# Performance work log

Measured on AMD Instinct MI355X. Metric: run time of the kernel, lower is better.

The kernel has to match this reference:

```python
import jax, jax.numpy as jnp
import numpy as np

N = 100000      # nodes
E = 3200000     # directed edges
G = 1024        # graphs in batch


def setup_inputs() -> dict:
    key = jax.random.key(0)
    ks = jax.random.split(key, 12)
    x = jax.random.normal(ks[0], (N, 4), dtype=jnp.float32)
    edge_index = jax.random.randint(ks[1], (2, E), 0, N, dtype=jnp.int64)
    batch = jnp.sort(jax.random.randint(ks[2], (N,), 0, G, dtype=jnp.int64))
    s = 0.1
    return {
        'x': x, 'edge_index': edge_index, 'batch': batch,
        'W_emb': jax.random.normal(ks[3], (4, 1), jnp.float32) * s,
        'b_emb': jax.random.normal(ks[4], (4,), jnp.float32) * s,
        'W1': jax.random.normal(ks[5], (16, 7), jnp.float32) * s,
        'b1': jax.random.normal(ks[6], (16,), jnp.float32) * s,
        'W2': jax.random.normal(ks[7], (8, 16), jnp.float32) * s,
        'b2': jax.random.normal(ks[8], (8,), jnp.float32) * s,
        'W3': jax.random.normal(ks[9], (1, 8), jnp.float32) * s,
        'b3': jax.random.normal(ks[10], (1,), jnp.float32) * s,
    }


def _gcn_norm(edge_index, n):
    # add self-loops (PyG GCNConv default)
    loops = jnp.arange(n, dtype=edge_index.dtype)
    row = jnp.concatenate([edge_index[0], loops])  # source
    col = jnp.concatenate([edge_index[1], loops])  # target
    deg = jax.ops.segment_sum(jnp.ones_like(col, dtype=jnp.float32), col, num_segments=n)
    dinv = jnp.where(deg > 0, deg ** -0.5, 0.0)
    norm = dinv[row] * dinv[col]
    return row, col, norm


def _gcn_conv(h, W, b, row, col, norm, n):
    h = h @ W.T                                   # [n, out]
    msg = h[row] * norm[:, None]                  # gather + scale
    out = jax.ops.segment_sum(msg, col, num_segments=n)
    return out + b


def reference(x, edge_index, batch, W_emb, b_emb, W1, b1, W2, b2, W3, b3):
    row, col, norm = _gcn_norm(edge_index, N)
    atoms_vector = x[:, :1]
    atoms_xyz = x[:, 1:]
    one_hot_emb = atoms_vector @ W_emb.T + b_emb          # [N, 4]
    h = jnp.concatenate([one_hot_emb, atoms_xyz], axis=1) # [N, 7]
    h = jnp.tanh(_gcn_conv(h, W1, b1, row, col, norm, N)) # [N, 16]
    # dropout is identity in eval mode
    h = jnp.tanh(_gcn_conv(h, W2, b2, row, col, norm, N)) # [N, 8]
    # scatter-mean readout over graphs
    sums = jax.ops.segment_sum(h, batch, num_segments=G)
    cnts = jax.ops.segment_sum(jnp.ones((h.shape[0],), h.dtype), batch, num_segments=G)
    pooled = sums / jnp.maximum(cnts, 1.0)[:, None]       # [G, 8]
    return pooled @ W3.T + b3                             # [G, 1]
```

## Files before the change

kernel.cpp:

```cpp
#include <hip/hip_runtime.h>
#include <hip/hip_fp16.h>


constexpr int BLK  = 256;
constexpr int NPB  = 256;
constexpr int NBMX = 512;
constexpr int CAPB = 9216;
constexpr int PBLK = 512;
constexpr int CAPS = 6144;
constexpr int EPT  = 12;
constexpr int SBLK = 512;
constexpr int NIT4 = 5;
constexpr float S8 = 64.0f;

__global__ void k_place(const int4* __restrict__ row4, const int4* __restrict__ col4,
                        int* __restrict__ bucketCnt, unsigned int* __restrict__ data,
                        int E, int NB) {
    __shared__ unsigned int stage[CAPS];
    __shared__ int pos[NBMX], sstart[NBMX], lbase[NBMX];
    __shared__ int wsum[8];
    int t = threadIdx.x;
    int lane = t & 63, w = t >> 6;
    int begin = blockIdx.x * CAPS;
    int end = min(E, begin + CAPS);
    int csize = end - begin;
    int q0 = begin >> 2, q1 = end >> 2;
    if (t < NBMX) pos[t] = 0;
    __syncthreads();
    unsigned int ent[EPT];
    int meta[EPT];
#pragma unroll
    for (int it = 0; it < EPT / 4; it++) {
        int i = q0 + t + it * PBLK;
        bool ok = i < q1;
        int4 c = ok ? col4[i] : make_int4(0, 0, 0, 0);
        int4 r = ok ? row4[i] : make_int4(0, 0, 0, 0);
#pragma unroll
        for (int k = 0; k < 4; k++) {
            int cc = ((const int*)&c)[k];
            int rr = ((const int*)&r)[k];
            int b = cc >> 8;
            int o = ok ? atomicAdd(&pos[b], 1) : 0;
            ent[it * 4 + k] = ((unsigned int)(cc & 255) << 17) | (unsigned int)rr;
            meta[it * 4 + k] = ok ? ((b << 13) | o) : -1;
        }
    }
    __syncthreads();
    int v = pos[t];
    int sc = v;
#pragma unroll
    for (int off = 1; off < 64; off <<= 1) {
        int o = __shfl_up(sc, off, 64);
        if (lane >= off) sc += o;
    }
    if (lane == 63) wsum[w] = sc;
    __syncthreads();
    int pre = 0;
#pragma unroll
    for (int i = 0; i < 8; i++) if (i < w) pre += wsum[i];
    int excl = sc + pre - v;
    sstart[t] = excl;
    lbase[t] = v ? atomicAdd(&bucketCnt[t], v) : 0;
    __syncthreads();
#pragma unroll
    for (int k = 0; k < EPT; k++) {
        int m = meta[k];
        if (m >= 0) stage[sstart[m >> 13] + (m & 0x1FFF)] = ent[k];
    }
    __syncthreads();
    for (int k = t; k < csize; k += PBLK) {
        int lo = 0, hi = NB - 1;
        while (lo < hi) { int m = (lo + hi + 1) >> 1; if (sstart[m] <= k) lo = m; else hi = m - 1; }
        data[(unsigned int)lo * CAPB + (unsigned int)(lbase[lo] + (k - sstart[lo]))] = stage[k];
    }
}

__global__ void k_sort_node1(unsigned int* __restrict__ data,
                             const int* __restrict__ bucketCnt,
                             const float4* __restrict__ x,
                             const float* __restrict__ Wemb, const float* __restrict__ bemb,
                             const float* __restrict__ W1,
                             int* __restrict__ rs, int* __restrict__ re,
                             float* __restrict__ dinv, uint4* __restrict__ u1q, int n) {
    __shared__ int pos[NPB], startl[NPB];
    __shared__ int wsum[4];
    int b = blockIdx.x;
    int t = threadIdx.x;
    int base = b * CAPB;
    int cnt = min(bucketCnt[b], CAPB);
    if (t < NPB) pos[t] = 0;
    __syncthreads();
    const uint4* data4 = (const uint4*)(data + base);
    unsigned int ent[NIT4 * 4];
    int off[NIT4 * 4];
#pragma unroll
    for (int it = 0; it < NIT4; it++) {
        int i4 = t + it * SBLK;
        int i = i4 * 4;
        uint4 p4 = (i < cnt) ? data4[i4] : make_uint4(0, 0, 0, 0);
#pragma unroll
        for (int k = 0; k < 4; k++) {
            int idx = it * 4 + k;
            if (i + k < cnt) {
                unsigned int p = ((const unsigned int*)&p4)[k];
                int dloc = (int)(p >> 17);
                int o = atomicAdd(&pos[dloc], 1);
                ent[idx] = p & 0x1FFFF;
                off[idx] = (dloc << 14) | o;
            } else off[idx] = -1;
        }
    }
    __syncthreads();
    int node = b * NPB + t;
    float d = 0.0f;
    if (t < NPB) {
        int lane = t & 63, w = t >> 6;
        int v = pos[t];
        int sc = v;
#pragma unroll
        for (int o = 1; o < 64; o <<= 1) {
            int s = __shfl_up(sc, o, 64);
            if (lane >= o) sc += s;
        }
        if (lane == 63) wsum[w] = sc;
        __syncthreads();
        int pre = 0;
#pragma unroll
        for (int i = 0; i < 4; i++) if (i < w) pre += wsum[i];
        int excl = sc + pre - v;
        startl[t] = excl;
        if (node < n) {
            rs[node] = base + excl;
            re[node] = base + excl + v;
            d = rsqrtf((float)v + 1.0f);
            dinv[node] = d;
        }
    } else {
        __syncthreads();
    }
    __syncthreads();
#pragma unroll
    for (int it = 0; it < NIT4 * 4; it++) {
        int m = off[it];
        if (m >= 0) data[base + startl[m >> 14] + (m & 0x3FFF)] = ent[it];
    }
    if (t < NPB && node < n) {
        float4 xi = x[node];
        float h0[7];
#pragma unroll
        for (int j = 0; j < 4; j++) h0[j] = xi.x * Wemb[j] + bemb[j];
        h0[4] = xi.y; h0[5] = xi.z; h0[6] = xi.w;
        float s[16];
#pragma unroll
        for (int f = 0; f < 16; f++) {
            float tt = 0.0f;
#pragma unroll
            for (int j = 0; j < 7; j++) tt += h0[j] * W1[f * 7 + j];
            s[f] = tt * d * S8;
        }
        unsigned int w0, w1, w2, w3;
        w0 = __builtin_amdgcn_cvt_pk_fp8_f32(s[0],  s[1],  0,  false);
        w0 = __builtin_amdgcn_cvt_pk_fp8_f32(s[2],  s[3],  w0, true);
        w1 = __builtin_amdgcn_cvt_pk_fp8_f32(s[4],  s[5],  0,  false);
        w1 = __builtin_amdgcn_cvt_pk_fp8_f32(s[6],  s[7],  w1, true);
        w2 = __builtin_amdgcn_cvt_pk_fp8_f32(s[8],  s[9],  0,  false);
        w2 = __builtin_amdgcn_cvt_pk_fp8_f32(s[10], s[11], w2, true);
        w3 = __builtin_amdgcn_cvt_pk_fp8_f32(s[12], s[13], 0,  false);
        w3 = __builtin_amdgcn_cvt_pk_fp8_f32(s[14], s[15], w3, true);
        u1q[node] = make_uint4(w0, w1, w2, w3);
    }
}

typedef float vfloat2 __attribute__((vector_size(8)));

__device__ __forceinline__ void dec16_add(uint4 q, float* acc) {
#pragma unroll
    for (int w = 0; w < 4; w++) {
        unsigned int u = ((const unsigned int*)&q)[w];
        vfloat2 lo = __builtin_amdgcn_cvt_pk_f32_fp8(u, false);
        vfloat2 hi = __builtin_amdgcn_cvt_pk_f32_fp8(u, true);
        acc[4 * w + 0] += lo[0]; acc[4 * w + 1] += lo[1];
        acc[4 * w + 2] += hi[0]; acc[4 * w + 3] += hi[1];
    }
}

__global__ void k_agg1(const unsigned int* __restrict__ sorted,
                       const int* __restrict__ rs, const int* __restrict__ re,
                       const uint4* __restrict__ u1q, const float* __restrict__ dinv,
                       const float* __restrict__ b1, const float* __restrict__ W2,
                       uint4* __restrict__ u2q, int n) {
    int node = blockIdx.x * BLK + threadIdx.x;
    if (node >= n) return;
    int s = rs[node], e = re[node];
    float acc[16];
#pragma unroll
    for (int k = 0; k < 16; k++) acc[k] = 0.0f;
    int i = s;
    for (; i + 4 <= e; i += 4) {
        uint4 q0 = u1q[sorted[i]];
        uint4 q1 = u1q[sorted[i + 1]];
        uint4 q2 = u1q[sorted[i + 2]];
        uint4 q3 = u1q[sorted[i + 3]];
        dec16_add(q0, acc);
        dec16_add(q1, acc);
        dec16_add(q2, acc);
        dec16_add(q3, acc);
    }
    for (; i < e; i++) {
        uint4 q = u1q[sorted[i]];
        dec16_add(q, acc);
    }
    uint4 qs = u1q[node];
    dec16_add(qs, acc);
    float d = dinv[node];
    float dS = d * (1.0f / S8);
    float h1[16];
#pragma unroll
    for (int k = 0; k < 16; k++) h1[k] = tanhf(dS * acc[k] + b1[k]);
    float r[8];
#pragma unroll
    for (int g = 0; g < 8; g++) {
        float tt = 0.0f;
#pragma unroll
        for (int k = 0; k < 16; k++) tt += h1[k] * W2[g * 16 + k];
        r[g] = tt * d;
    }
    union { __half2 h2[4]; uint4 u4; } pk;
#pragma unroll
    for (int q = 0; q < 4; q++) pk.h2[q] = __floats2half2_rn(r[2 * q], r[2 * q + 1]);
    u2q[node] = pk.u4;
}

__global__ void k_agg2_pool(const unsigned int* __restrict__ sorted,
                            const int* __restrict__ rs, const int* __restrict__ re,
                            const uint4* __restrict__ u2q, const float* __restrict__ dinv,
                            const float* __restrict__ b2, const int* __restrict__ batch,
                            float* __restrict__ pooled, float* __restrict__ cnt, int n) {
    int node = blockIdx.x * BLK + threadIdx.x;
    int lane = threadIdx.x & 63;
    bool valid = node < n;
    float h[8];
#pragma unroll
    for (int k = 0; k < 8; k++) h[k] = 0.0f;
    int g = -1;
    if (valid) {
        int s = rs[node], e = re[node];
        float acc[8];
#pragma unroll
        for (int k = 0; k < 8; k++) acc[k] = 0.0f;
        int i = s;
        for (; i + 2 <= e; i += 2) {
            uint4 q0 = u2q[sorted[i]];
            uint4 q1 = u2q[sorted[i + 1]];
            const __half2* p0 = (const __half2*)&q0;
            const __half2* p1 = (const __half2*)&q1;
#pragma unroll
            for (int k = 0; k < 4; k++) {
                float2 a0 = __half22float2(p0[k]);
                float2 a1 = __half22float2(p1[k]);
                acc[2*k]   += a0.x + a1.x;
                acc[2*k+1] += a0.y + a1.y;
            }
        }
        if (i < e) {
            uint4 q = u2q[sorted[i]];
            const __half2* p = (const __half2*)&q;
#pragma unroll
            for (int k = 0; k < 4; k++) {
                float2 a = __half22float2(p[k]);
                acc[2*k]   += a.x;
                acc[2*k+1] += a.y;
            }
        }
        uint4 qs = u2q[node];
        const __half2* ps = (const __half2*)&qs;
        float d = dinv[node];
#pragma unroll
        for (int k = 0; k < 4; k++) {
            float2 a = __half22float2(ps[k]);
            h[2*k]   = tanhf(d * (acc[2*k]   + a.x) + b2[2*k]);
            h[2*k+1] = tanhf(d * (acc[2*k+1] + a.y) + b2[2*k+1]);
        }
        g = batch[node];
    }
    float c = valid ? 1.0f : 0.0f;
#pragma unroll
    for (int off = 1; off < 64; off <<= 1) {
        int gn = __shfl_down(g, off, 64);
        float cn = __shfl_down(c, off, 64);
        float hn[8];
#pragma unroll
        for (int k = 0; k < 8; k++) hn[k] = __shfl_down(h[k], off, 64);
        bool take = (lane + off < 64) && (gn == g);
        if (take) {
            c += cn;
#pragma unroll
            for (int k = 0; k < 8; k++) h[k] += hn[k];
        }
    }
    int gprev = __shfl_up(g, 1, 64);
    bool head = valid && (lane == 0 || gprev != g);
    if (head) {
#pragma unroll
        for (int k = 0; k < 8; k++) atomicAdd(&pooled[g * 8 + k], h[k]);
        atomicAdd(&cnt[g], c);
    }
}

__global__ void k_out(const float* __restrict__ pooled, const float* __restrict__ cnt,
                      const float* __restrict__ W3, const float* __restrict__ b3,
                      float* __restrict__ out, int G) {
    int g = blockIdx.x * BLK + threadIdx.x;
    if (g >= G) return;
    float c = fmaxf(cnt[g], 1.0f);
    float t = 0.0f;
#pragma unroll
    for (int k = 0; k < 8; k++) t += pooled[g * 8 + k] * W3[k];
    out[g] = t / c + b3[0];
}

extern "C" void kernel_launch(void* const* d_in, const int* in_sizes, int n_in,
                              void* d_out, int out_size, void* d_ws, size_t ws_size,
                              hipStream_t stream) {
    const float* x    = (const float*)d_in[0];
    const int*   ei   = (const int*)d_in[1];
    const int*   batch= (const int*)d_in[2];
    const float* Wemb = (const float*)d_in[3];
    const float* bemb = (const float*)d_in[4];
    const float* W1   = (const float*)d_in[5];
    const float* b1   = (const float*)d_in[6];
    const float* W2   = (const float*)d_in[7];
    const float* b2   = (const float*)d_in[8];
    const float* W3   = (const float*)d_in[9];
    const float* b3   = (const float*)d_in[10];
    float* out = (float*)d_out;

    const int n = in_sizes[2];
    const int E = in_sizes[1] / 2;
    const int G = out_size;
    const int* row = ei;
    const int* col = ei + E;
    const int NB = (n + NPB - 1) / NPB;

    float* ws    = (float*)d_ws;
    float* dinv  = ws;
    uint4* u1q   = (uint4*)(ws + n);
    __half* u2h  = (__half*)(ws + 9 * n);
    int* rs      = (int*)(ws + 13 * n);
    int* re      = rs + n;
    int* bucketCnt = re + n;
    float* pooled  = (float*)(bucketCnt + NBMX);
    float* cnt     = pooled + 8 * G;
    unsigned int* data = (unsigned int*)(cnt + G);

    int gridP = (E + CAPS - 1) / CAPS;

    hipMemsetAsync(bucketCnt, 0, (NBMX + 8 * G + G) * sizeof(int), stream);
    k_place<<<gridP, PBLK, 0, stream>>>((const int4*)row, (const int4*)col,
                                        bucketCnt, data, E, NB);
    k_sort_node1<<<NB, SBLK, 0, stream>>>(data, bucketCnt, (const float4*)x,
                                          Wemb, bemb, W1, rs, re, dinv, u1q, n);
    k_agg1<<<(n + BLK - 1) / BLK, BLK, 0, stream>>>(data, rs, re, u1q,
                                                    dinv, b1, W2, (uint4*)u2h, n);
    k_agg2_pool<<<(n + BLK - 1) / BLK, BLK, 0, stream>>>(data, rs, re,
                                                         (const uint4*)u2h, dinv, b2,
                                                         batch, pooled, cnt, n);
    k_out<<<(G + BLK - 1) / BLK, BLK, 0, stream>>>(pooled, cnt, W3, b3, out, G);
}
```

Baseline: 191.7 us.

## Split each node's neighbor aggregation across four lanes with shuffle reduction

Both aggregation kernels now assign four threads per node. Each thread strides over every fourth incoming edge, and the partial sums are combined with xor-shuffles. This spreads long edge lists across more threads, raising memory-level parallelism and reducing per-thread latency chains, at the cost of four times as many threads, duplicated per-node tail math (tanh and W2 matvec in agg1), and more shuffle traffic. The pooling segmented reduction now starts at offset 4 and only lane-group leaders contribute.

```diff
diff --git a/kernel.cpp b/kernel.cpp
--- a/kernel.cpp
+++ b/kernel.cpp
@@ -189,29 +189,34 @@
                        const uint4* __restrict__ u1q, const float* __restrict__ dinv,
                        const float* __restrict__ b1, const float* __restrict__ W2,
                        uint4* __restrict__ u2q, int n) {
-    int node = blockIdx.x * BLK + threadIdx.x;
+    int tt = blockIdx.x * BLK + threadIdx.x;
+    int node = tt >> 2;
+    int j = tt & 3;
     if (node >= n) return;
     int s = rs[node], e = re[node];
     float acc[16];
 #pragma unroll
     for (int k = 0; k < 16; k++) acc[k] = 0.0f;
-    int i = s;
-    for (; i + 4 <= e; i += 4) {
+    int i = s + j;
+    for (; i + 4 < e; i += 8) {
         uint4 q0 = u1q[sorted[i]];
-        uint4 q1 = u1q[sorted[i + 1]];
-        uint4 q2 = u1q[sorted[i + 2]];
-        uint4 q3 = u1q[sorted[i + 3]];
+        uint4 q1 = u1q[sorted[i + 4]];
         dec16_add(q0, acc);
         dec16_add(q1, acc);
-        dec16_add(q2, acc);
-        dec16_add(q3, acc);
-    }
-    for (; i < e; i++) {
+    }
+    if (i < e) {
         uint4 q = u1q[sorted[i]];
         dec16_add(q, acc);
     }
-    uint4 qs = u1q[node];
-    dec16_add(qs, acc);
+    if (j == 0) {
+        uint4 qs = u1q[node];
+        dec16_add(qs, acc);
+    }
+#pragma unroll
+    for (int k = 0; k < 16; k++) {
+        acc[k] += __shfl_xor(acc[k], 1, 64);
+        acc[k] += __shfl_xor(acc[k], 2, 64);
+    }
     float d = dinv[node];
     float dS = d * (1.0f / S8);
     float h1[16];
@@ -220,15 +225,17 @@
     float r[8];
 #pragma unroll
     for (int g = 0; g < 8; g++) {
-        float tt = 0.0f;
-#pragma unroll
-        for (int k = 0; k < 16; k++) tt += h1[k] * W2[g * 16 + k];
-        r[g] = tt * d;
-    }
-    union { __half2 h2[4]; uint4 u4; } pk;
-#pragma unroll
-    for (int q = 0; q < 4; q++) pk.h2[q] = __floats2half2_rn(r[2 * q], r[2 * q + 1]);
-    u2q[node] = pk.u4;
+        float ttv = 0.0f;
+#pragma unroll
+        for (int k = 0; k < 16; k++) ttv += h1[k] * W2[g * 16 + k];
+        r[g] = ttv * d;
+    }
+    if (j == 0) {
+        union { __half2 h2[4]; uint4 u4; } pk;
+#pragma unroll
+        for (int q = 0; q < 4; q++) pk.h2[q] = __floats2half2_rn(r[2 * q], r[2 * q + 1]);
+        u2q[node] = pk.u4;
+    }
 }
 
 __global__ void k_agg2_pool(const unsigned int* __restrict__ sorted,
@@ -236,22 +243,25 @@
                             const uint4* __restrict__ u2q, const float* __restrict__ dinv,
                             const float* __restrict__ b2, const int* __restrict__ batch,
                             float* __restrict__ pooled, float* __restrict__ cnt, int n) {
-    int node = blockIdx.x * BLK + threadIdx.x;
+    int tt = blockIdx.x * BLK + threadIdx.x;
+    int node = tt >> 2;
+    int j = tt & 3;
     int lane = threadIdx.x & 63;
     bool valid = node < n;
     float h[8];
 #pragma unroll
     for (int k = 0; k < 8; k++) h[k] = 0.0f;
     int g = -1;
+    float c = 0.0f;
     if (valid) {
         int s = rs[node], e = re[node];
         float acc[8];
 #pragma unroll
         for (int k = 0; k < 8; k++) acc[k] = 0.0f;
-        int i = s;
-        for (; i + 2 <= e; i += 2) {
+        int i = s + j;
+        for (; i + 4 < e; i += 8) {
             uint4 q0 = u2q[sorted[i]];
-            uint4 q1 = u2q[sorted[i + 1]];
+            uint4 q1 = u2q[sorted[i + 4]];
             const __half2* p0 = (const __half2*)&q0;
             const __half2* p1 = (const __half2*)&q1;
 #pragma unroll
@@ -272,20 +282,31 @@
                 acc[2*k+1] += a.y;
             }
         }
-        uint4 qs = u2q[node];
-        const __half2* ps = (const __half2*)&qs;
-        float d = dinv[node];
-#pragma unroll
-        for (int k = 0; k < 4; k++) {
-            float2 a = __half22float2(ps[k]);
-            h[2*k]   = tanhf(d * (acc[2*k]   + a.x) + b2[2*k]);
-            h[2*k+1] = tanhf(d * (acc[2*k+1] + a.y) + b2[2*k+1]);
-        }
-        g = batch[node];
-    }
-    float c = valid ? 1.0f : 0.0f;
-#pragma unroll
-    for (int off = 1; off < 64; off <<= 1) {
+        if (j == 0) {
+            uint4 qs = u2q[node];
+            const __half2* ps = (const __half2*)&qs;
+#pragma unroll
+            for (int k = 0; k < 4; k++) {
+                float2 a = __half22float2(ps[k]);
+                acc[2*k]   += a.x;
+                acc[2*k+1] += a.y;
+            }
+        }
+#pragma unroll
+        for (int k = 0; k < 8; k++) {
+            acc[k] += __shfl_xor(acc[k], 1, 64);
+            acc[k] += __shfl_xor(acc[k], 2, 64);
+        }
+        if (j == 0) {
+            float d = dinv[node];
+#pragma unroll
+            for (int k = 0; k < 8; k++) h[k] = tanhf(d * acc[k] + b2[k]);
+            g = batch[node];
+            c = 1.0f;
+        }
+    }
+#pragma unroll
+    for (int off = 4; off < 64; off <<= 1) {
         int gn = __shfl_down(g, off, 64);
         float cn = __shfl_down(c, off, 64);
         float hn[8];
@@ -298,8 +319,8 @@
             for (int k = 0; k < 8; k++) h[k] += hn[k];
         }
     }
-    int gprev = __shfl_up(g, 1, 64);
-    bool head = valid && (lane == 0 || gprev != g);
+    int gprev = __shfl_up(g, 4, 64);
+    bool head = valid && (j == 0) && (lane == 0 || gprev != g);
     if (head) {
 #pragma unroll
         for (int k = 0; k < 8; k++) atomicAdd(&pooled[g * 8 + k], h[k]);
@@ -354,16 +375,17 @@
     unsigned int* data = (unsigned int*)(cnt + G);
 
     int gridP = (E + CAPS - 1) / CAPS;
+    int gridA = (4 * n + BLK - 1) / BLK;
 
     hipMemsetAsync(bucketCnt, 0, (NBMX + 8 * G + G) * sizeof(int), stream);
     k_place<<<gridP, PBLK, 0, stream>>>((const int4*)row, (const int4*)col,
                                         bucketCnt, data, E, NB);
     k_sort_node1<<<NB, SBLK, 0, stream>>>(data, bucketCnt, (const float4*)x,
                                           Wemb, bemb, W1, rs, re, dinv, u1q, n);
-    k_agg1<<<(n + BLK - 1) / BLK, BLK, 0, stream>>>(data, rs, re, u1q,
-                                                    dinv, b1, W2, (uint4*)u2h, n);
-    k_agg2_pool<<<(n + BLK - 1) / BLK, BLK, 0, stream>>>(data, rs, re,
-                                                         (const uint4*)u2h, dinv, b2,
-                                                         batch, pooled, cnt, n);
+    k_agg1<<<gridA, BLK, 0, stream>>>(data, rs, re, u1q,
+                                      dinv, b1, W2, (uint4*)u2h, n);
+    k_agg2_pool<<<gridA, BLK, 0, stream>>>(data, rs, re,
+                                           (const uint4*)u2h, dinv, b2,
+                                           batch, pooled, cnt, n);
     k_out<<<(G + BLK - 1) / BLK, BLK, 0, stream>>>(pooled, cnt, W3, b3, out, G);
 }
```

After: 189.5 us. Within noise of the previous version (-1.2%).
